# Performance work log

Measured on AMD Instinct MI355X. Metric: run time of the kernel, lower is better.

## Reference

```python
import jax, jax.numpy as jnp
import numpy as np

N = 100000        # nodes
E = 1600000       # edges
DES, TWEET, NUMP, CATP = 768, 768, 6, 11
IN_DIM, H, R = 512, 128, 2
BR = IN_DIM // 4  # per-branch width = 128


def setup_inputs() -> dict:
    key = jax.random.key(0)
    ks = jax.random.split(key, 16)
    w = lambda k, s: jax.random.normal(k, s, jnp.float32) * 0.02
    z = lambda d: jnp.zeros((d,), jnp.float32)
    return {
        "x": jax.random.normal(ks[0], (N, NUMP + TWEET + CATP + DES), jnp.float32),
        "edge_index": jax.random.randint(ks[1], (2, E), 0, N),
        "edge_type": jax.random.randint(ks[2], (E,), 0, R),
        "W_des": w(ks[3], (DES, BR)),   "b_des": z(BR),
        "W_tweet": w(ks[4], (TWEET, BR)), "b_tweet": z(BR),
        "W_num": w(ks[5], (NUMP, BR)),  "b_num": z(BR),
        "W_cat": w(ks[6], (CATP, BR)),  "b_cat": z(BR),
        "W_in": w(ks[7], (IN_DIM, H)),  "b_in": z(H),
        "prelu_a": jnp.full((H,), 0.25, jnp.float32),
        "root1": w(ks[8], (H, H)), "rel1": w(ks[9], (R, H, H)), "bias1": z(H),
        "root2": w(ks[10], (H, H)), "rel2": w(ks[11], (R, H, H)), "bias2": z(H),
        "W_cls": w(ks[12], (H, H)), "b_cls": z(H),
    }


def _leaky(v):
    return jnp.where(v >= 0, v, 0.01 * v)


def _rgcn(h, src, dst, edge_type, root, rel_w, bias):
    # PyG RGCNConv (default mean aggregation per relation):
    # out_i = bias + h_i @ root + sum_r mean_{j in N_r(i)} h_j @ W_r
    out = h @ root + bias
    for r in range(R):  # R is small and fixed
        mask = (edge_type == r).astype(h.dtype)          # [E]
        msg = (h @ rel_w[r])[src] * mask[:, None]        # [E, H]
        agg = jax.ops.segment_sum(msg, dst, num_segments=N)
        cnt = jax.ops.segment_sum(mask, dst, num_segments=N)
        out = out + agg / jnp.maximum(cnt, 1.0)[:, None]
    return out


def reference(x, edge_index, edge_type,
              W_des, b_des, W_tweet, b_tweet, W_num, b_num, W_cat, b_cat,
              W_in, b_in, prelu_a,
              root1, rel1, bias1, root2, rel2, bias2, W_cls, b_cls):
    # feature column layout: [num_prop | tweet | cat_prop | des]
    num_prop = x[:, :NUMP]
    tweet = x[:, NUMP:NUMP + TWEET]
    cat_prop = x[:, NUMP + TWEET:NUMP + TWEET + CATP]
    des = x[:, NUMP + TWEET + CATP:]

    d = _leaky(des @ W_des + b_des)
    t = _leaky(tweet @ W_tweet + b_tweet)
    n = _leaky(num_prop @ W_num + b_num)
    c = _leaky(cat_prop @ W_cat + b_cat)
    h = jnp.concatenate((d, t, n, c), axis=1) @ W_in + b_in
    h = jnp.where(h >= 0, h, prelu_a * h)  # PReLU, per-channel alpha

    src, dst = edge_index[0], edge_index[1]
    h = _rgcn(h, src, dst, edge_type, root1, rel1, bias1)
    h = _rgcn(h, src, dst, edge_type, root2, rel2, bias2)
    return h @ W_cls + b_cls
```

## Files before the change

kernel.cpp:

```cpp
#include <hip/hip_runtime.h>
#include <cstdint>
#include <cstddef>

#define NN 100000
#define EE 1600000
#define XDIM 1553
#define HD 128

typedef __attribute__((ext_vector_type(8))) short short8;
typedef __attribute__((ext_vector_type(4))) float f32x4;
typedef float f32x4u __attribute__((vector_size(16), aligned(4)));

union Frag { unsigned int u[4]; short8 s; uint4 v; };

#define OFF_DES_HI 0
#define OFF_DES_LO 98304
#define OFF_TW_HI  196608
#define OFF_TW_LO  294912
#define OFF_NUM_HI 393216
#define OFF_NUM_LO 397312
#define OFF_CAT_HI 401408
#define OFF_CAT_LO 405504
#define OFF_WIN_HI 409600
#define OFF_WIN_LO 475136
#define OFF_L1_HI  540672
#define OFF_L1_LO  589824
#define OFF_L2_HI  638976
#define OFF_L2_LO  688128
#define OFF_CLS_HI 737280
#define OFF_CLS_LO 753664
#define WT_SITES   385024

__device__ __forceinline__ void cvt_pair(float f0, float f1,
                                         unsigned int& hi, unsigned int& lo) {
  unsigned int u0 = __float_as_uint(f0), u1 = __float_as_uint(f1);
  hi = __builtin_amdgcn_perm(u1, u0, 0x07060302u);
  float l0 = f0 - __uint_as_float(u0 & 0xFFFF0000u);
  float l1 = f1 - __uint_as_float(u1 & 0xFFFF0000u);
  lo = __builtin_amdgcn_perm(__float_as_uint(l1), __float_as_uint(l0), 0x07060302u);
}

__device__ __forceinline__ void fence_barrier() {
  asm volatile("" ::: "memory");
  __builtin_amdgcn_s_barrier();
  asm volatile("" ::: "memory");
}
__device__ __forceinline__ void lgkm0_barrier() {
  asm volatile("s_waitcnt lgkmcnt(0)" ::: "memory");
  __builtin_amdgcn_s_barrier();
  asm volatile("" ::: "memory");
}

__global__ __launch_bounds__(256) void k_prepw(
    const float* __restrict__ Wdes, const float* __restrict__ Wtw,
    const float* __restrict__ Wnum, const float* __restrict__ Wcat,
    const float* __restrict__ Win,  const float* __restrict__ root1,
    const float* __restrict__ rel1, const float* __restrict__ root2,
    const float* __restrict__ rel2, const float* __restrict__ Wcls,
    unsigned short* __restrict__ Wt) {
  int id = blockIdx.x * 256 + threadIdx.x;
  if (id >= WT_SITES) return;
  const float* src; int K, Kpad, dhi, dlo, local;
  if (id < 98304)       { src=Wdes;        K=768; Kpad=768; dhi=OFF_DES_HI;       dlo=OFF_DES_LO;       local=id; }
  else if (id < 196608) { src=Wtw;         K=768; Kpad=768; dhi=OFF_TW_HI;        dlo=OFF_TW_LO;        local=id-98304; }
  else if (id < 200704) { src=Wnum;        K=6;   Kpad=32;  dhi=OFF_NUM_HI;       dlo=OFF_NUM_LO;       local=id-196608; }
  else if (id < 204800) { src=Wcat;        K=11;  Kpad=32;  dhi=OFF_CAT_HI;       dlo=OFF_CAT_LO;       local=id-200704; }
  else if (id < 270336) { src=Win;         K=512; Kpad=512; dhi=OFF_WIN_HI;       dlo=OFF_WIN_LO;       local=id-204800; }
  else if (id < 286720) { src=root1;       K=128; Kpad=128; dhi=OFF_L1_HI;        dlo=OFF_L1_LO;        local=id-270336; }
  else if (id < 303104) { src=rel1;        K=128; Kpad=128; dhi=OFF_L1_HI+16384;  dlo=OFF_L1_LO+16384;  local=id-286720; }
  else if (id < 319488) { src=rel1+16384;  K=128; Kpad=128; dhi=OFF_L1_HI+32768;  dlo=OFF_L1_LO+32768;  local=id-303104; }
  else if (id < 335872) { src=root2;       K=128; Kpad=128; dhi=OFF_L2_HI;        dlo=OFF_L2_LO;        local=id-319488; }
  else if (id < 352256) { src=rel2;        K=128; Kpad=128; dhi=OFF_L2_HI+16384;  dlo=OFF_L2_LO+16384;  local=id-335872; }
  else if (id < 368640) { src=rel2+16384;  K=128; Kpad=128; dhi=OFF_L2_HI+32768;  dlo=OFF_L2_LO+32768;  local=id-352256; }
  else                  { src=Wcls;        K=128; Kpad=128; dhi=OFF_CLS_HI;       dlo=OFF_CLS_LO;       local=id-368640; }
  int col = local / Kpad;
  int k = local - col * Kpad;
  float v = (k < K) ? src[(size_t)k * 128 + col] : 0.f;
  unsigned int u = __float_as_uint(v);
  float lo = v - __uint_as_float(u & 0xFFFF0000u);
  Wt[dhi + col * Kpad + k] = (unsigned short)(u >> 16);
  Wt[dlo + col * Kpad + k] = (unsigned short)(__float_as_uint(lo) >> 16);
}

__global__ __launch_bounds__(128) void k_fusew(
    const float* __restrict__ root2, const float* __restrict__ rel2,
    const float* __restrict__ Wcls,  const float* __restrict__ bias2,
    const float* __restrict__ bcls,  unsigned short* __restrict__ Wt,
    float* __restrict__ bfused) {
  int k = blockIdx.x;
  int c = threadIdx.x;
  const float* wrow;
  if (k < 128)      wrow = root2 + (size_t)k * 128;
  else if (k < 256) wrow = rel2 + (size_t)(k - 128) * 128;
  else if (k < 384) wrow = rel2 + 16384 + (size_t)(k - 256) * 128;
  else              wrow = bias2;
  float s = 0.f;
  for (int j = 0; j < 128; ++j) s += wrow[j] * Wcls[(size_t)j * 128 + c];
  if (k == 384) { bfused[c] = s + bcls[c]; return; }
  unsigned int u = __float_as_uint(s);
  float lo = s - __uint_as_float(u & 0xFFFF0000u);
  int sub = k >> 7, kl = k & 127;
  Wt[OFF_L2_HI + sub * 16384 + c * 128 + kl] = (unsigned short)(u >> 16);
  Wt[OFF_L2_LO + sub * 16384 + c * 128 + kl] = (unsigned short)(__float_as_uint(lo) >> 16);
}

__global__ __launch_bounds__(256) void k_count(const int* __restrict__ ei,
                                               const int* __restrict__ et,
                                               int* __restrict__ cnt2) {
  int e = blockIdx.x * 256 + threadIdx.x;
  if (e >= EE) return;
  atomicAdd(&cnt2[et[e] * NN + ei[EE + e]], 1);
}

__global__ __launch_bounds__(256) void k_scan1(const int* __restrict__ cnt2,
                                               int* __restrict__ row_ptr,
                                               int* __restrict__ bsum) {
  __shared__ int sums[256];
  int t = threadIdx.x;
  int base = blockIdx.x * 1024 + t * 4;
  int v[4]; int s = 0;
#pragma unroll
  for (int j = 0; j < 4; ++j) {
    int idx = base + j;
    v[j] = (idx < NN) ? (cnt2[idx] + cnt2[NN + idx]) : 0;
    s += v[j];
  }
  sums[t] = s;
  __syncthreads();
  for (int d = 1; d < 256; d <<= 1) {
    int val = (t >= d) ? sums[t - d] : 0;
    __syncthreads();
    sums[t] += val;
    __syncthreads();
  }
  int excl = sums[t] - s;
  if (t == 255) bsum[blockIdx.x] = sums[t];
  int run = excl;
#pragma unroll
  for (int j = 0; j < 4; ++j) {
    int idx = base + j;
    if (idx < NN) row_ptr[idx] = run;
    run += v[j];
  }
}

__global__ __launch_bounds__(128) void k_scan2(int* __restrict__ bsum, int nb) {
  __shared__ int s[128];
  int t = threadIdx.x;
  int v = (t < nb) ? bsum[t] : 0;
  s[t] = v;
  __syncthreads();
  for (int d = 1; d < 128; d <<= 1) {
    int val = (t >= d) ? s[t - d] : 0;
    __syncthreads();
    s[t] += val;
    __syncthreads();
  }
  if (t < nb) bsum[t] = s[t] - v;
}

__global__ __launch_bounds__(256) void k_scan3(int* __restrict__ row_ptr,
                                               const int* __restrict__ bsum) {
  int idx = blockIdx.x * 256 + threadIdx.x;
  if (idx < NN) row_ptr[idx] += bsum[idx >> 10];
  if (idx == NN) row_ptr[NN] = EE;
}

__global__ __launch_bounds__(256) void k_fill(const int* __restrict__ ei,
                                              const int* __restrict__ et,
                                              const int* __restrict__ row_ptr,
                                              int* __restrict__ fillpos,
                                              int* __restrict__ entries) {
  int e = blockIdx.x * 256 + threadIdx.x;
  if (e >= EE) return;
  int src = ei[e];
  int dst = ei[EE + e];
  int r = et[e];
  int pos = atomicAdd(&fillpos[dst], 1);
  entries[row_ptr[dst] + pos] = src | (r << 20);
}

__global__ __launch_bounds__(256, 3) void k_proj2(
    const float* __restrict__ x,
    const float* __restrict__ bdes, const float* __restrict__ btw,
    const float* __restrict__ bnum, const float* __restrict__ bcat,
    const float* __restrict__ bin,  const float* __restrict__ pa,
    const unsigned short* __restrict__ Wt, float* __restrict__ h0) {
  __shared__ unsigned short bt_hi[128 * 32], bt_lo[128 * 32];
  __shared__ unsigned short z_hi[64 * 128], z_lo[64 * 128];

  const int t = threadIdx.x;
  const int node0 = blockIdx.x * 64;
  const int w = t >> 6, lane = t & 63;
  const int li = lane & 15, lg = lane >> 4;

  const int cr0 = t >> 2, c0 = t & 3;
  const int cr1 = cr0 + 64;
  const unsigned stb0 = cr0 * 64 + ((c0 ^ ((cr0 >> 1) & 3)) << 4);
  const unsigned stb1 = cr1 * 64 + ((c0 ^ ((cr1 >> 1) & 3)) << 4);

  const int rowA = w * 16 + li;
  int nodeA = node0 + rowA;
  int ndA = nodeA < NN ? nodeA : NN - 1;
  const float* xrow = x + (size_t)ndA * XDIM;

#define STORE_BT(SH0, SL0, SH1, SL1)              \
  do {                                            \
    *(uint4*)((char*)bt_hi + stb0) = (SH0);       \
    *(uint4*)((char*)bt_lo + stb0) = (SL0);       \
    *(uint4*)((char*)bt_hi + stb1) = (SH1);       \
    *(uint4*)((char*)bt_lo + stb1) = (SL1);       \
  } while (0)

#define CVT_A2(FA, FB, AH, AL)                                                   \
  do {                                                                           \
    cvt_pair((FA)[0], (FA)[1], (AH).u[0], (AL).u[0]);                            \
    cvt_pair((FA)[2], (FA)[3], (AH).u[1], (AL).u[1]);                            \
    cvt_pair((FB)[0], (FB)[1], (AH).u[2], (AL).u[2]);                            \
    cvt_pair((FB)[2], (FB)[3], (AH).u[3], (AL).u[3]);                            \
  } while (0)

#define MFMA8(AH, AL, ACC)                                                       \
  do {                                                                           \
    _Pragma("unroll")                                                            \
    for (int ct_ = 0; ct_ < 8; ++ct_) {                                          \
      int colrow_ = ct_ * 16 + li;                                               \
      int byte_ = colrow_ * 64 + (lg << 4);                                      \
      byte_ ^= ((colrow_ >> 1) & 3) << 4;                                        \
      Frag bh_, bl_;                                                             \
      bh_.v = *(const uint4*)((char*)bt_hi + byte_);                             \
      bl_.v = *(const uint4*)((char*)bt_lo + byte_);                             \
      (ACC)[ct_] = __builtin_amdgcn_mfma_f32_16x16x32_bf16((AH).s, bl_.s, (ACC)[ct_], 0, 0, 0); \
      (ACC)[ct_] = __builtin_amdgcn_mfma_f32_16x16x32_bf16((AL).s, bh_.s, (ACC)[ct_], 0, 0, 0); \
      (ACC)[ct_] = __builtin_amdgcn_mfma_f32_16x16x32_bf16((AH).s, bh_.s, (ACC)[ct_], 0, 0, 0); \
    }                                                                            \
  } while (0)

#define TILE(WC0, WC1, WC2, WC3, WN0, WN1, WN2, WN3, XA, XB, T)                  \
  do {                                                                           \
    STORE_BT(WC0, WC1, WC2, WC3);                                                \
    lgkm0_barrier();                                                             \
    Frag ah_, al_;                                                               \
    CVT_A2(XA, XB, ah_, al_);                                                    \
    {                                                                            \
      const int kw_ = ((T) + 1) * 32;                                            \
      WN0 = *(const uint4*)(ph0 + kw_); WN1 = *(const uint4*)(pl0 + kw_);        \
      WN2 = *(const uint4*)(ph1 + kw_); WN3 = *(const uint4*)(pl1 + kw_);        \
      int kx_ = (T) + 3; if (kx_ > 23) kx_ = 23; kx_ *= 32;                      \
      XA = *(const f32x4u*)(xr + kx_);                                           \
      XB = *(const f32x4u*)(xr + kx_ + 4);                                       \
    }                                                                            \
    MFMA8(ah_, al_, zacc);                                                       \
    fence_barrier();                                                             \
  } while (0)

#define MFMA_B(KT)                                                               \
  do {                                                                           \
    Frag ah_, al_;                                                               \
    int byte_ = rowA * 256 + (((KT) * 32 + lg * 8) << 1);                        \
    byte_ ^= (rowA & 7) << 4;                                                    \
    ah_.v = *(const uint4*)((char*)z_hi + byte_);                                \
    al_.v = *(const uint4*)((char*)z_lo + byte_);                                \
    MFMA8(ah_, al_, hacc);                                                       \
  } while (0)

#define Z_EPI(ZACC, BIASP)                                                       \
  do {                                                                           \
    _Pragma("unroll")                                                            \
    for (int ct_ = 0; ct_ < 8; ++ct_) {                                          \
      int col_ = ct_ * 16 + li;                                                  \
      float bv_ = (BIASP)[col_];                                                 \
      _Pragma("unroll")                                                          \
      for (int r_ = 0; r_ < 4; ++r_) {                                           \
        float v_ = (ZACC)[ct_][r_] + bv_;                                        \
        v_ = v_ >= 0.f ? v_ : 0.01f * v_;                                        \
        int row_ = w * 16 + lg * 4 + r_;                                         \
        int byte_ = row_ * 256 + col_ * 2;                                       \
        byte_ ^= (row_ & 7) << 4;                                                \
        unsigned int u_ = __float_as_uint(v_);                                   \
        *(unsigned short*)((char*)z_hi + byte_) = (unsigned short)(u_ >> 16);    \
        float lo_ = v_ - __uint_as_float(u_ & 0xFFFF0000u);                      \
        *(unsigned short*)((char*)z_lo + byte_) = (unsigned short)(__float_as_uint(lo_) >> 16); \
      }                                                                          \
    }                                                                            \
  } while (0)

#define PHASE_B(SLICE)                                                           \
  do {                                                                           \
    const unsigned short* qh0_ = Wt + OFF_WIN_HI + cr0 * 512 + (SLICE) * 128 + c0 * 8; \
    const unsigned short* ql0_ = Wt + OFF_WIN_LO + cr0 * 512 + (SLICE) * 128 + c0 * 8; \
    const unsigned short* qh1_ = Wt + OFF_WIN_HI + cr1 * 512 + (SLICE) * 128 + c0 * 8; \
    const unsigned short* ql1_ = Wt + OFF_WIN_LO + cr1 * 512 + (SLICE) * 128 + c0 * 8; \
    uint4 wA0_ = *(const uint4*)(qh0_), wA1_ = *(const uint4*)(ql0_);            \
    uint4 wA2_ = *(const uint4*)(qh1_), wA3_ = *(const uint4*)(ql1_);            \
    uint4 wB0_, wB1_, wB2_, wB3_;                                                \
    STORE_BT(wA0_, wA1_, wA2_, wA3_);                                            \
    lgkm0_barrier();                                                             \
    wB0_ = *(const uint4*)(qh0_ + 32); wB1_ = *(const uint4*)(ql0_ + 32);        \
    wB2_ = *(const uint4*)(qh1_ + 32); wB3_ = *(const uint4*)(ql1_ + 32);        \
    MFMA_B(0);                                                                   \
    fence_barrier();                                                             \
    STORE_BT(wB0_, wB1_, wB2_, wB3_);                                            \
    lgkm0_barrier();                                                             \
    wA0_ = *(const uint4*)(qh0_ + 64); wA1_ = *(const uint4*)(ql0_ + 64);        \
    wA2_ = *(const uint4*)(qh1_ + 64); wA3_ = *(const uint4*)(ql1_ + 64);        \
    MFMA_B(1);                                                                   \
    fence_barrier();                                                             \
    STORE_BT(wA0_, wA1_, wA2_, wA3_);                                            \
    lgkm0_barrier();                                                             \
    wB0_ = *(const uint4*)(qh0_ + 96); wB1_ = *(const uint4*)(ql0_ + 96);        \
    wB2_ = *(const uint4*)(qh1_ + 96); wB3_ = *(const uint4*)(ql1_ + 96);        \
    MFMA_B(2);                                                                   \
    fence_barrier();                                                             \
    STORE_BT(wB0_, wB1_, wB2_, wB3_);                                            \
    lgkm0_barrier();                                                             \
    MFMA_B(3);                                                                   \
    fence_barrier();                                                             \
  } while (0)

  f32x4 hacc[8];
#pragma unroll
  for (int b = 0; b < 8; ++b) hacc[b] = (f32x4)0.f;

#pragma unroll
  for (int s = 0; s < 2; ++s) {
    const int off = (s == 0) ? 785 : 6;
    const unsigned short* wh = Wt + (s == 0 ? OFF_DES_HI : OFF_TW_HI);
    const unsigned short* wl = Wt + (s == 0 ? OFF_DES_LO : OFF_TW_LO);
    const float* bias = (s == 0) ? bdes : btw;

    const float* xr = xrow + off + lg * 8;
    const unsigned short* ph0 = wh + cr0 * 768 + c0 * 8;
    const unsigned short* pl0 = wl + cr0 * 768 + c0 * 8;
    const unsigned short* ph1 = wh + cr1 * 768 + c0 * 8;
    const unsigned short* pl1 = wl + cr1 * 768 + c0 * 8;

    f32x4 zacc[8];
#pragma unroll
    for (int b = 0; b < 8; ++b) zacc[b] = (f32x4)0.f;

    uint4 WA0, WA1, WA2, WA3, WB0, WB1, WB2, WB3;
    f32x4u X0a, X0b, X1a, X1b, X2a, X2b;

    WA0 = *(const uint4*)(ph0); WA1 = *(const uint4*)(pl0);
    WA2 = *(const uint4*)(ph1); WA3 = *(const uint4*)(pl1);
    X0a = *(const f32x4u*)(xr);      X0b = *(const f32x4u*)(xr + 4);
    X1a = *(const f32x4u*)(xr + 32); X1b = *(const f32x4u*)(xr + 36);
    X2a = *(const f32x4u*)(xr + 64); X2b = *(const f32x4u*)(xr + 68);

    for (int base = 0; base < 24; base += 6) {
      TILE(WA0, WA1, WA2, WA3, WB0, WB1, WB2, WB3, X0a, X0b, base + 0);
      TILE(WB0, WB1, WB2, WB3, WA0, WA1, WA2, WA3, X1a, X1b, base + 1);
      TILE(WA0, WA1, WA2, WA3, WB0, WB1, WB2, WB3, X2a, X2b, base + 2);
      TILE(WB0, WB1, WB2, WB3, WA0, WA1, WA2, WA3, X0a, X0b, base + 3);
      TILE(WA0, WA1, WA2, WA3, WB0, WB1, WB2, WB3, X1a, X1b, base + 4);
      TILE(WB0, WB1, WB2, WB3, WA0, WA1, WA2, WA3, X2a, X2b, base + 5);
    }
    Z_EPI(zacc, bias);
    PHASE_B(s);
  }

#pragma unroll
  for (int u = 0; u < 2; ++u) {
    const int offu = (u == 0) ? 0 : 774;
    const int Ksu = (u == 0) ? 6 : 11;
    const unsigned short* wh = Wt + (u == 0 ? OFF_NUM_HI : OFF_CAT_HI);
    const unsigned short* wl = Wt + (u == 0 ? OFF_NUM_LO : OFF_CAT_LO);
    const float* biasu = (u == 0) ? bnum : bcat;
    const float* xr = xrow + offu + lg * 8;

    uint4 s0 = *(const uint4*)(wh + cr0 * 32 + c0 * 8);
    uint4 s1 = *(const uint4*)(wl + cr0 * 32 + c0 * 8);
    uint4 s2 = *(const uint4*)(wh + cr1 * 32 + c0 * 8);
    uint4 s3 = *(const uint4*)(wl + cr1 * 32 + c0 * 8);
    f32x4u fa = *(const f32x4u*)(xr);
    f32x4u fb = *(const f32x4u*)(xr + 4);
#pragma unroll
    for (int j = 0; j < 4; ++j) {
      if (lg * 8 + j >= Ksu) fa[j] = 0.f;
      if (lg * 8 + 4 + j >= Ksu) fb[j] = 0.f;
    }

    f32x4 zacc[8];
#pragma unroll
    for (int b = 0; b < 8; ++b) zacc[b] = (f32x4)0.f;

    STORE_BT(s0, s1, s2, s3);
    lgkm0_barrier();
    {
      Frag ah_, al_;
      CVT_A2(fa, fb, ah_, al_);
      MFMA8(ah_, al_, zacc);
    }
    fence_barrier();
    Z_EPI(zacc, biasu);
    PHASE_B(u + 2);
  }

#pragma unroll
  for (int ct = 0; ct < 8; ++ct) {
    int col = ct * 16 + li;
    float bi = bin[col];
    float p = pa[col];
#pragma unroll
    for (int r = 0; r < 4; ++r) {
      int node = node0 + w * 16 + lg * 4 + r;
      if (node < NN) {
        float v = hacc[ct][r] + bi;
        v = v >= 0.f ? v : p * v;
        h0[(size_t)node * HD + col] = v;
      }
    }
  }

#undef TILE
#undef MFMA_B
#undef Z_EPI
#undef PHASE_B
}

__global__ __launch_bounds__(256) void k_gather(
    const float* __restrict__ h, float* __restrict__ aggH,
    const int* __restrict__ row_ptr, const int* __restrict__ cnt2,
    const int* __restrict__ entries) {
  int i = blockIdx.x * 4 + (threadIdx.x >> 6);
  int l = threadIdx.x & 63;
  if (i >= NN) return;
  int rs = row_ptr[i], re = row_ptr[i + 1];
  int c0 = cnt2[i], c1 = cnt2[NN + i];
  float inv0 = 1.f / (float)(c0 > 0 ? c0 : 1);
  float inv1 = 1.f / (float)(c1 > 0 ? c1 : 1);
  float a0 = 0, a1 = 0, b0 = 0, b1 = 0;
  int e = rs;
  for (; e + 1 < re; e += 2) {
    int ent0 = entries[e], ent1 = entries[e + 1];
    const float2* r0 = (const float2*)(h + (size_t)(ent0 & 0xFFFFF) * HD);
    const float2* r1 = (const float2*)(h + (size_t)(ent1 & 0xFFFFF) * HD);
    float2 v0 = r0[l], v1 = r1[l];
    if (ent0 >> 20) { b0 += v0.x; b1 += v0.y; } else { a0 += v0.x; a1 += v0.y; }
    if (ent1 >> 20) { b0 += v1.x; b1 += v1.y; } else { a0 += v1.x; a1 += v1.y; }
  }
  if (e < re) {
    int ent = entries[e];
    const float2* r0 = (const float2*)(h + (size_t)(ent & 0xFFFFF) * HD);
    float2 v0 = r0[l];
    if (ent >> 20) { b0 += v0.x; b1 += v0.y; } else { a0 += v0.x; a1 += v0.y; }
  }
  float2* p0 = (float2*)(aggH + (size_t)i * HD);
  float2* p1 = (float2*)(aggH + (size_t)NN * HD + (size_t)i * HD);
  p0[l] = make_float2(a0 * inv0, a1 * inv0);
  p1[l] = make_float2(b0 * inv1, b1 * inv1);
}

__global__ __launch_bounds__(256, 4) void k_rgemm2(
    const float* __restrict__ hin, const float* __restrict__ aggH,
    const unsigned short* __restrict__ wl_hi, const unsigned short* __restrict__ wl_lo,
    const float* __restrict__ bias, float* __restrict__ outp) {
  __shared__ unsigned short bt_hi[128 * 32], bt_lo[128 * 32];

  const int t = threadIdx.x;
  const int node0 = blockIdx.x * 64;
  const int w = t >> 6, lane = t & 63;
  const int li = lane & 15, lg = lane >> 4;

  const int cr0 = t >> 2, c0 = t & 3;
  const int cr1 = cr0 + 64;
  const unsigned stb0 = cr0 * 64 + ((c0 ^ ((cr0 >> 1) & 3)) << 4);
  const unsigned stb1 = cr1 * 64 + ((c0 ^ ((cr1 >> 1) & 3)) << 4);

  const int rowA = w * 16 + li;
  int nodeA = node0 + rowA;
  int ndA = nodeA < NN ? nodeA : NN - 1;
  const float* a0p = hin + (size_t)ndA * HD + lg * 8;
  const float* a1p = aggH + (size_t)ndA * HD + lg * 8;
  const float* a2p = aggH + (size_t)NN * HD + (size_t)ndA * HD + lg * 8;

#define W2H(KT, CR) (wl_hi + ((KT) >> 2) * 16384 + (CR) * 128 + ((KT) & 3) * 32 + c0 * 8)
#define W2L(KT, CR) (wl_lo + ((KT) >> 2) * 16384 + (CR) * 128 + ((KT) & 3) * 32 + c0 * 8)

#define TILE2(WC0, WC1, WC2, WC3, WN0, WN1, WN2, WN3, XA, XB, T)                 \
  do {                                                                           \
    STORE_BT(WC0, WC1, WC2, WC3);                                                \
    lgkm0_barrier();                                                             \
    Frag ah_, al_;                                                               \
    CVT_A2(XA, XB, ah_, al_);                                                    \
    {                                                                            \
      int kn_ = (T) + 1; if (kn_ > 11) kn_ = 11;                                 \
      WN0 = *(const uint4*)W2H(kn_, cr0); WN1 = *(const uint4*)W2L(kn_, cr0);    \
      WN2 = *(const uint4*)W2H(kn_, cr1); WN3 = *(const uint4*)W2L(kn_, cr1);    \
      int kx_ = (T) + 3; if (kx_ > 11) kx_ = 11;                                 \
      const float* ap_ = (kx_ < 4) ? a0p : (kx_ < 8) ? a1p : a2p;                \
      XA = *(const f32x4u*)(ap_ + (kx_ & 3) * 32);                               \
      XB = *(const f32x4u*)(ap_ + (kx_ & 3) * 32 + 4);                           \
    }                                                                            \
    MFMA8(ah_, al_, acc);                                                        \
    fence_barrier();                                                             \
  } while (0)

  f32x4 acc[8];
#pragma unroll
  for (int b = 0; b < 8; ++b) acc[b] = (f32x4)0.f;

  uint4 WA0, WA1, WA2, WA3, WB0, WB1, WB2, WB3;
  f32x4u X0a, X0b, X1a, X1b, X2a, X2b;

  WA0 = *(const uint4*)W2H(0, cr0); WA1 = *(const uint4*)W2L(0, cr0);
  WA2 = *(const uint4*)W2H(0, cr1); WA3 = *(const uint4*)W2L(0, cr1);
  X0a = *(const f32x4u*)(a0p);      X0b = *(const f32x4u*)(a0p + 4);
  X1a = *(const f32x4u*)(a0p + 32); X1b = *(const f32x4u*)(a0p + 36);
  X2a = *(const f32x4u*)(a0p + 64); X2b = *(const f32x4u*)(a0p + 68);

  TILE2(WA0, WA1, WA2, WA3, WB0, WB1, WB2, WB3, X0a, X0b, 0);
  TILE2(WB0, WB1, WB2, WB3, WA0, WA1, WA2, WA3, X1a, X1b, 1);
  TILE2(WA0, WA1, WA2, WA3, WB0, WB1, WB2, WB3, X2a, X2b, 2);
  TILE2(WB0, WB1, WB2, WB3, WA0, WA1, WA2, WA3, X0a, X0b, 3);
  TILE2(WA0, WA1, WA2, WA3, WB0, WB1, WB2, WB3, X1a, X1b, 4);
  TILE2(WB0, WB1, WB2, WB3, WA0, WA1, WA2, WA3, X2a, X2b, 5);
  TILE2(WA0, WA1, WA2, WA3, WB0, WB1, WB2, WB3, X0a, X0b, 6);
  TILE2(WB0, WB1, WB2, WB3, WA0, WA1, WA2, WA3, X1a, X1b, 7);
  TILE2(WA0, WA1, WA2, WA3, WB0, WB1, WB2, WB3, X2a, X2b, 8);
  TILE2(WB0, WB1, WB2, WB3, WA0, WA1, WA2, WA3, X0a, X0b, 9);
  TILE2(WA0, WA1, WA2, WA3, WB0, WB1, WB2, WB3, X1a, X1b, 10);
  TILE2(WB0, WB1, WB2, WB3, WA0, WA1, WA2, WA3, X2a, X2b, 11);

#pragma unroll
  for (int ct = 0; ct < 8; ++ct) {
    int col = ct * 16 + li;
    float bv = bias[col];
#pragma unroll
    for (int r = 0; r < 4; ++r) {
      int node = node0 + w * 16 + lg * 4 + r;
      if (node < NN) outp[(size_t)node * HD + col] = acc[ct][r] + bv;
    }
  }

#undef W2H
#undef W2L
#undef TILE2
}

extern "C" void kernel_launch(void* const* d_in, const int* in_sizes, int n_in,
                              void* d_out, int out_size, void* d_ws, size_t ws_size,
                              hipStream_t stream) {
  const float* x    = (const float*)d_in[0];
  const int* ei     = (const int*)d_in[1];
  const int* et     = (const int*)d_in[2];
  const float* Wdes = (const float*)d_in[3];
  const float* bdes = (const float*)d_in[4];
  const float* Wtw  = (const float*)d_in[5];
  const float* btw  = (const float*)d_in[6];
  const float* Wnum = (const float*)d_in[7];
  const float* bnum = (const float*)d_in[8];
  const float* Wcat = (const float*)d_in[9];
  const float* bcat = (const float*)d_in[10];
  const float* Win  = (const float*)d_in[11];
  const float* bin  = (const float*)d_in[12];
  const float* pa   = (const float*)d_in[13];
  const float* root1 = (const float*)d_in[14];
  const float* rel1  = (const float*)d_in[15];
  const float* bias1 = (const float*)d_in[16];
  const float* root2 = (const float*)d_in[17];
  const float* rel2  = (const float*)d_in[18];
  const float* bias2 = (const float*)d_in[19];
  const float* Wcls  = (const float*)d_in[20];
  const float* bcls  = (const float*)d_in[21];
  float* out = (float*)d_out;

  char* p = (char*)d_ws;
  float* aggH = (float*)p;    p += (size_t)2 * NN * HD * 4;
  float* hB = (float*)p;      p += (size_t)NN * HD * 4;
  int* row_ptr = (int*)p;     p += ((size_t)NN + 4) * 4;
  int* cnt2 = (int*)p;        p += (size_t)2 * NN * 4;
  int* fillpos = (int*)p;     p += (size_t)NN * 4;
  int* entries = (int*)p;     p += (size_t)EE * 4;
  int* bsum = (int*)p;        p += 512;
  float* bfused = (float*)p;  p += 512;
  unsigned short* Wt = (unsigned short*)p;  p += (size_t)WT_SITES * 2 * 2;

  k_prepw<<<(WT_SITES + 255) / 256, 256, 0, stream>>>(
      Wdes, Wtw, Wnum, Wcat, Win, root1, rel1, root2, rel2, Wcls, Wt);
  k_fusew<<<385, 128, 0, stream>>>(root2, rel2, Wcls, bias2, bcls, Wt, bfused);

  hipMemsetAsync(cnt2, 0, (size_t)3 * NN * 4, stream);
  k_count<<<EE / 256, 256, 0, stream>>>(ei, et, cnt2);
  int nb = (NN + 1023) / 1024;
  k_scan1<<<nb, 256, 0, stream>>>(cnt2, row_ptr, bsum);
  k_scan2<<<1, 128, 0, stream>>>(bsum, nb);
  k_scan3<<<(NN + 1 + 255) / 256, 256, 0, stream>>>(row_ptr, bsum);
  k_fill<<<EE / 256, 256, 0, stream>>>(ei, et, row_ptr, fillpos, entries);

  const int nblk = (NN + 63) / 64;
  k_proj2<<<nblk, 256, 0, stream>>>(x, bdes, btw, bnum, bcat, bin, pa, Wt, out);
  k_gather<<<NN / 4, 256, 0, stream>>>(out, aggH, row_ptr, cnt2, entries);
  k_rgemm2<<<nblk, 256, 0, stream>>>(out, aggH, Wt + OFF_L1_HI, Wt + OFF_L1_LO,
                                     bias1, hB);
  k_gather<<<NN / 4, 256, 0, stream>>>(hB, aggH, row_ptr, cnt2, entries);
  k_rgemm2<<<nblk, 256, 0, stream>>>(hB, aggH, Wt + OFF_L2_HI, Wt + OFF_L2_LO,
                                     bfused, out);
}
```

Before: 946.1 us.

## Merge edge count into weight prep, fill into projection, unroll gather by four

Folds the edge-count atomics into the weight-preparation launch as extra blocks, and folds the CSR fill into the projection GEMM launch as extra trailing blocks, so the independent work overlaps and fewer kernels are launched. The neighbor gather loop is unrolled from two to four edges per iteration to keep more row loads in flight. The risk is that the fill blocks share a launch with the heavy GEMM blocks and so inherit its LDS and occupancy limits, which lowers how many fill blocks can run at once.

```diff
diff --git a/kernel.cpp b/kernel.cpp
--- a/kernel.cpp
+++ b/kernel.cpp
@@ -31,6 +31,11 @@
 #define OFF_CLS_LO 753664
 #define WT_SITES   385024
 
+#define PREPW_BLOCKS 1504
+#define COUNT_BLOCKS 6250
+#define PROJ_NBLK    1563
+#define FILL_BLOCKS  6250
+
 __device__ __forceinline__ void cvt_pair(float f0, float f1,
                                          unsigned int& hi, unsigned int& lo) {
   unsigned int u0 = __float_as_uint(f0), u1 = __float_as_uint(f1);
@@ -51,13 +56,20 @@
   asm volatile("" ::: "memory");
 }
 
-__global__ __launch_bounds__(256) void k_prepw(
+__global__ __launch_bounds__(256) void k_setup(
     const float* __restrict__ Wdes, const float* __restrict__ Wtw,
     const float* __restrict__ Wnum, const float* __restrict__ Wcat,
     const float* __restrict__ Win,  const float* __restrict__ root1,
     const float* __restrict__ rel1, const float* __restrict__ root2,
     const float* __restrict__ rel2, const float* __restrict__ Wcls,
-    unsigned short* __restrict__ Wt) {
+    unsigned short* __restrict__ Wt,
+    const int* __restrict__ ei, const int* __restrict__ et,
+    int* __restrict__ cnt2) {
+  if (blockIdx.x >= PREPW_BLOCKS) {
+    int e = (blockIdx.x - PREPW_BLOCKS) * 256 + threadIdx.x;
+    if (e < EE) atomicAdd(&cnt2[et[e] * NN + ei[EE + e]], 1);
+    return;
+  }
   int id = blockIdx.x * 256 + threadIdx.x;
   if (id >= WT_SITES) return;
   const float* src; int K, Kpad, dhi, dlo, local;
@@ -104,14 +116,6 @@
   Wt[OFF_L2_LO + sub * 16384 + c * 128 + kl] = (unsigned short)(__float_as_uint(lo) >> 16);
 }
 
-__global__ __launch_bounds__(256) void k_count(const int* __restrict__ ei,
-                                               const int* __restrict__ et,
-                                               int* __restrict__ cnt2) {
-  int e = blockIdx.x * 256 + threadIdx.x;
-  if (e >= EE) return;
-  atomicAdd(&cnt2[et[e] * NN + ei[EE + e]], 1);
-}
-
 __global__ __launch_bounds__(256) void k_scan1(const int* __restrict__ cnt2,
                                                int* __restrict__ row_ptr,
                                                int* __restrict__ bsum) {
@@ -166,28 +170,29 @@
   if (idx == NN) row_ptr[NN] = EE;
 }
 
-__global__ __launch_bounds__(256) void k_fill(const int* __restrict__ ei,
-                                              const int* __restrict__ et,
-                                              const int* __restrict__ row_ptr,
-                                              int* __restrict__ fillpos,
-                                              int* __restrict__ entries) {
-  int e = blockIdx.x * 256 + threadIdx.x;
-  if (e >= EE) return;
-  int src = ei[e];
-  int dst = ei[EE + e];
-  int r = et[e];
-  int pos = atomicAdd(&fillpos[dst], 1);
-  entries[row_ptr[dst] + pos] = src | (r << 20);
-}
-
 __global__ __launch_bounds__(256, 3) void k_proj2(
     const float* __restrict__ x,
     const float* __restrict__ bdes, const float* __restrict__ btw,
     const float* __restrict__ bnum, const float* __restrict__ bcat,
     const float* __restrict__ bin,  const float* __restrict__ pa,
-    const unsigned short* __restrict__ Wt, float* __restrict__ h0) {
+    const unsigned short* __restrict__ Wt, float* __restrict__ h0,
+    const int* __restrict__ ei, const int* __restrict__ et,
+    const int* __restrict__ row_ptr, int* __restrict__ fillpos,
+    int* __restrict__ entries) {
   __shared__ unsigned short bt_hi[128 * 32], bt_lo[128 * 32];
   __shared__ unsigned short z_hi[64 * 128], z_lo[64 * 128];
+
+  if (blockIdx.x >= PROJ_NBLK) {
+    int e = (blockIdx.x - PROJ_NBLK) * 256 + threadIdx.x;
+    if (e < EE) {
+      int src = ei[e];
+      int dst = ei[EE + e];
+      int r = et[e];
+      int pos = atomicAdd(&fillpos[dst], 1);
+      entries[row_ptr[dst] + pos] = src | (r << 20);
+    }
+    return;
+  }
 
   const int t = threadIdx.x;
   const int node0 = blockIdx.x * 64;
@@ -432,15 +437,20 @@
   float inv1 = 1.f / (float)(c1 > 0 ? c1 : 1);
   float a0 = 0, a1 = 0, b0 = 0, b1 = 0;
   int e = rs;
-  for (; e + 1 < re; e += 2) {
+  for (; e + 3 < re; e += 4) {
     int ent0 = entries[e], ent1 = entries[e + 1];
+    int ent2 = entries[e + 2], ent3 = entries[e + 3];
     const float2* r0 = (const float2*)(h + (size_t)(ent0 & 0xFFFFF) * HD);
     const float2* r1 = (const float2*)(h + (size_t)(ent1 & 0xFFFFF) * HD);
-    float2 v0 = r0[l], v1 = r1[l];
+    const float2* r2 = (const float2*)(h + (size_t)(ent2 & 0xFFFFF) * HD);
+    const float2* r3 = (const float2*)(h + (size_t)(ent3 & 0xFFFFF) * HD);
+    float2 v0 = r0[l], v1 = r1[l], v2 = r2[l], v3 = r3[l];
     if (ent0 >> 20) { b0 += v0.x; b1 += v0.y; } else { a0 += v0.x; a1 += v0.y; }
     if (ent1 >> 20) { b0 += v1.x; b1 += v1.y; } else { a0 += v1.x; a1 += v1.y; }
-  }
-  if (e < re) {
+    if (ent2 >> 20) { b0 += v2.x; b1 += v2.y; } else { a0 += v2.x; a1 += v2.y; }
+    if (ent3 >> 20) { b0 += v3.x; b1 += v3.y; } else { a0 += v3.x; a1 += v3.y; }
+  }
+  for (; e < re; ++e) {
     int ent = entries[e];
     const float2* r0 = (const float2*)(h + (size_t)(ent & 0xFFFFF) * HD);
     float2 v0 = r0[l];
@@ -577,24 +587,24 @@
   float* bfused = (float*)p;  p += 512;
   unsigned short* Wt = (unsigned short*)p;  p += (size_t)WT_SITES * 2 * 2;
 
-  k_prepw<<<(WT_SITES + 255) / 256, 256, 0, stream>>>(
-      Wdes, Wtw, Wnum, Wcat, Win, root1, rel1, root2, rel2, Wcls, Wt);
+  (void)hipMemsetAsync(cnt2, 0, (size_t)3 * NN * 4, stream);
+  k_setup<<<PREPW_BLOCKS + COUNT_BLOCKS, 256, 0, stream>>>(
+      Wdes, Wtw, Wnum, Wcat, Win, root1, rel1, root2, rel2, Wcls, Wt,
+      ei, et, cnt2);
   k_fusew<<<385, 128, 0, stream>>>(root2, rel2, Wcls, bias2, bcls, Wt, bfused);
 
-  hipMemsetAsync(cnt2, 0, (size_t)3 * NN * 4, stream);
-  k_count<<<EE / 256, 256, 0, stream>>>(ei, et, cnt2);
   int nb = (NN + 1023) / 1024;
   k_scan1<<<nb, 256, 0, stream>>>(cnt2, row_ptr, bsum);
   k_scan2<<<1, 128, 0, stream>>>(bsum, nb);
   k_scan3<<<(NN + 1 + 255) / 256, 256, 0, stream>>>(row_ptr, bsum);
-  k_fill<<<EE / 256, 256, 0, stream>>>(ei, et, row_ptr, fillpos, entries);
-
-  const int nblk = (NN + 63) / 64;
-  k_proj2<<<nblk, 256, 0, stream>>>(x, bdes, btw, bnum, bcat, bin, pa, Wt, out);
+
+  k_proj2<<<PROJ_NBLK + FILL_BLOCKS, 256, 0, stream>>>(
+      x, bdes, btw, bnum, bcat, bin, pa, Wt, out,
+      ei, et, row_ptr, fillpos, entries);
   k_gather<<<NN / 4, 256, 0, stream>>>(out, aggH, row_ptr, cnt2, entries);
-  k_rgemm2<<<nblk, 256, 0, stream>>>(out, aggH, Wt + OFF_L1_HI, Wt + OFF_L1_LO,
-                                     bias1, hB);
+  k_rgemm2<<<PROJ_NBLK, 256, 0, stream>>>(out, aggH, Wt + OFF_L1_HI, Wt + OFF_L1_LO,
+                                          bias1, hB);
   k_gather<<<NN / 4, 256, 0, stream>>>(hB, aggH, row_ptr, cnt2, entries);
-  k_rgemm2<<<nblk, 256, 0, stream>>>(hB, aggH, Wt + OFF_L2_HI, Wt + OFF_L2_LO,
-                                     bfused, out);
-}
+  k_rgemm2<<<PROJ_NBLK, 256, 0, stream>>>(hB, aggH, Wt + OFF_L2_HI, Wt + OFF_L2_LO,
+                                          bfused, out);
+}
```

New measurement: 896.4 us. -5.2%, faster.
